# Kernel optimization log

Hardware: AMD Instinct MI355X
Metric: run time of the kernel (lower is better)

Reference implementation:

```python
import jax, jax.numpy as jnp
import numpy as np

LP, LQ, B, D0, H = 128, 128, 64, 150, 150
D = 2 * D0  # in_size after self-concatenation


def setup_inputs() -> dict:
    key = jax.random.key(0)
    ks = jax.random.split(key, 12)
    s = 0.08  # weight scale to keep tanh/sigmoid out of hard saturation
    return {
        "Up": jax.random.normal(ks[0], (LP, B, D0), jnp.float32),
        "Uq": jax.random.normal(ks[1], (LQ, B, D0), jnp.float32),
        "Wp": jax.random.normal(ks[2], (H, D), jnp.float32) * s,
        "Wq": jax.random.normal(ks[3], (H, D), jnp.float32) * s,
        "Wv": jax.random.normal(ks[4], (H, H), jnp.float32) * s,
        "Wg": jax.random.normal(ks[5], (2 * D, 2 * D), jnp.float32) * s,
        "V": jax.random.normal(ks[6], (B, H), jnp.float32) * s,
        "v0": jax.random.normal(ks[7], (B, H), jnp.float32) * s,
        "W_ih": jax.random.normal(ks[8], (3 * H, 2 * D), jnp.float32) * s,
        "W_hh": jax.random.normal(ks[9], (3 * H, H), jnp.float32) * s,
        "b_ih": jax.random.normal(ks[10], (3 * H,), jnp.float32) * s,
        "b_hh": jax.random.normal(ks[11], (3 * H,), jnp.float32) * s,
    }


def reference(Up, Uq, Wp, Wq, Wv, Wg, V, v0, W_ih, W_hh, b_ih, b_hh):
    # self-concat of features, as in the original forward
    Upc = jnp.concatenate([Up, Up], axis=2)  # (LP, B, D)
    Uqc = jnp.concatenate([Uq, Uq], axis=2)  # (LQ, B, D)
    # Wq @ Uq is loop-invariant in the original; hoist it (same math)
    Wuq = jnp.einsum('lbd,hd->lbh', Uqc, Wq)  # (LQ, B, H)

    def step(v, up_i):
        # up_i: (B, D); v: (B, H)
        wup = up_i @ Wp.T                                   # (B, H)
        x = jnp.tanh(wup[None] + Wuq + (v @ Wv.T)[None])    # (LQ, B, H)
        s = jnp.einsum('lbh,bh->bl', x, V)                  # (B, LQ)
        a = jax.nn.softmax(s, axis=1)
        c = jnp.einsum('bl,lbd->bd', a, Uqc)                # (B, D)
        r = jnp.concatenate([up_i, c], axis=1)              # (B, 2D)
        r = jax.nn.sigmoid(r @ Wg.T) * r                    # gated input
        # PyTorch GRUCell math
        gi = r @ W_ih.T + b_ih                              # (B, 3H)
        gh = v @ W_hh.T + b_hh                              # (B, 3H)
        i_r, i_z, i_n = jnp.split(gi, 3, axis=1)
        h_r, h_z, h_n = jnp.split(gh, 3, axis=1)
        rr = jax.nn.sigmoid(i_r + h_r)
        zz = jax.nn.sigmoid(i_z + h_z)
        n = jnp.tanh(i_n + rr * h_n)
        h = (1.0 - zz) * n + zz * v
        return h, h

    _, vs = jax.lax.scan(step, v0, Upc)  # vs: (LP, B, H)
    return vs  # dropout in eval mode = identity
```

## Files before the change

kernel.cpp:

```cpp
#include <hip/hip_runtime.h>
#include <hip/hip_fp16.h>

typedef _Float16 h2_t __attribute__((ext_vector_type(2)));

__device__ __forceinline__ float dot2f(int w, int x, float acc) {
#if __has_builtin(__builtin_amdgcn_fdot2)
  return __builtin_amdgcn_fdot2(__builtin_bit_cast(h2_t, w),
                                __builtin_bit_cast(h2_t, x), acc, false);
#else
  h2_t a = __builtin_bit_cast(h2_t, w);
  h2_t b = __builtin_bit_cast(h2_t, x);
  return acc + (float)a[0] * (float)b[0] + (float)a[1] * (float)b[1];
#endif
}

__device__ __forceinline__ float rcp_f(float x) {
#if __has_builtin(__builtin_amdgcn_rcpf)
  return __builtin_amdgcn_rcpf(x);
#else
  return 1.0f / x;
#endif
}

__device__ __forceinline__ float fast_tanh(float x) {
  float e = exp2f(x * 2.885390082f);
  return 1.0f - 2.0f * rcp_f(e + 1.0f);
}
__device__ __forceinline__ float fast_sigmoid(float x) {
  return rcp_f(1.0f + exp2f(x * -1.442695041f));
}
__device__ __forceinline__ int packh2(float a, float b) {
  h2_t h;
  h[0] = (_Float16)a;
  h[1] = (_Float16)b;
  return __builtin_bit_cast(int, h);
}

__device__ __forceinline__ int ldi_coh(const int* p) {
  return __hip_atomic_load((int*)p, __ATOMIC_RELAXED, __HIP_MEMORY_SCOPE_AGENT);
}
__device__ __forceinline__ float ldf_coh(const float* p) {
  return __hip_atomic_load((float*)p, __ATOMIC_RELAXED,
                           __HIP_MEMORY_SCOPE_AGENT);
}
__device__ __forceinline__ void sti_coh(int* p, int v) {
  __hip_atomic_store(p, v, __ATOMIC_RELAXED, __HIP_MEMORY_SCOPE_AGENT);
}
__device__ __forceinline__ void stf_coh(float* p, float v) {
  __hip_atomic_store(p, v, __ATOMIC_RELAXED, __HIP_MEMORY_SCOPE_AGENT);
}

#define DOTC(W, X, A)                                                          \
  {                                                                            \
    int4 _x = (X);                                                             \
    A = dot2f((W).x, _x.x, A);                                                 \
    A = dot2f((W).y, _x.y, A);                                                 \
    A = dot2f((W).z, _x.z, A);                                                 \
    A = dot2f((W).w, _x.w, A);                                                 \
  }

__global__ void prep_weights(const float* __restrict__ Wp,
                             const float* __restrict__ Wv,
                             const float* __restrict__ Wg,
                             const float* __restrict__ Wih,
                             const float* __restrict__ Whh,
                             __half* __restrict__ oMa, __half* __restrict__ oWg,
                             __half* __restrict__ oWih,
                             __half* __restrict__ oWhh, int* __restrict__ flags,
                             int* __restrict__ payload) {
  if (blockIdx.x == 0) {
    for (int j = threadIdx.x; j < 1024; j += 256) flags[j] = 0;
  }
  if (blockIdx.x == 1 && threadIdx.x < 384) {
    int cc = threadIdx.x / 6, s = threadIdx.x % 6;
    int off;
    if (s < 2)
      off = 150 + s;
    else if (s < 4)
      off = 160 + 150 + (s - 2);
    else
      off = 160 + 302 + (s - 4);
    payload[cc * 2048 + off] = 0;
  }
  int idx = blockIdx.x * 256 + threadIdx.x;
  const int NMa = 150 * 304, NWg = 600 * 304, NWih = 900 * 304,
            NWhh = 452 * 152;
  if (idx < NMa) {
    int r = idx / 304, c = idx % 304;
    float v = 0.f;
    if (c < 150)
      v = Wp[r * 300 + c] + Wp[r * 300 + 150 + c];
    else if (c >= 152 && c < 302)
      v = Wv[r * 150 + (c - 152)];
    oMa[(c >> 3) * 1200 + r * 8 + (c & 7)] = __float2half(v);
    return;
  }
  idx -= NMa;
  if (idx < NWg) {
    int r = idx / 304, c = idx % 304;
    float v = 0.f;
    if (c < 150)
      v = Wg[r * 600 + c] + Wg[r * 600 + 150 + c];
    else if (c >= 152 && c < 302) {
      int d = c - 152;
      v = Wg[r * 600 + 300 + d] + Wg[r * 600 + 450 + d];
    }
    oWg[(c >> 3) * 4800 + r * 8 + (c & 7)] = __float2half(v);
    return;
  }
  idx -= NWg;
  if (idx < NWih) {
    int s = idx / 304, c = idx % 304;
    int r = s >> 1, off = (s & 1) * 300;
    float v = (c < 300) ? Wih[r * 600 + off + c] : 0.f;
    oWih[(c >> 3) * 7200 + s * 8 + (c & 7)] = __float2half(v);
    return;
  }
  idx -= NWih;
  if (idx < NWhh) {
    int r = idx / 152, c = idx % 152;
    float v = (r < 450 && c < 150) ? Whh[r * 150 + c] : 0.f;
    oWhh[(c >> 3) * 3616 + r * 8 + (c & 7)] = __float2half(v);
  }
}

__global__ __launch_bounds__(256) void prep_wuq(const float* __restrict__ Uq,
                                                const float* __restrict__ Wq,
                                                __half* __restrict__ oWuq,
                                                __half* __restrict__ oUqh) {
  __shared__ float sUql[64 * 150];
  const int l = blockIdx.x, tid = threadIdx.x;
  for (int idx = tid; idx < 9600; idx += 256) sUql[idx] = Uq[l * 9600 + idx];
  __syncthreads();
  for (int idx = tid; idx < 64 * 152; idx += 256) {
    int bb = idx / 152, d = idx % 152;
    float v = (d < 150) ? sUql[bb * 150 + d] : 0.f;
    oUqh[(size_t)bb * 19456 + l * 152 + d] = __float2half(v);
  }
  if (tid < 152) {
    const int h = tid;
    if (h < 150) {
      float wq[150];
#pragma unroll
      for (int d = 0; d < 150; ++d)
        wq[d] = Wq[h * 300 + d] + Wq[h * 300 + 150 + d];
      for (int bb = 0; bb < 64; ++bb) {
        float acc = 0.f;
#pragma unroll
        for (int d = 0; d < 150; ++d) acc += wq[d] * sUql[bb * 150 + d];
        oWuq[(size_t)bb * 19456 + l * 152 + h] = __float2half(acc);
      }
    } else {
      for (int bb = 0; bb < 64; ++bb)
        oWuq[(size_t)bb * 19456 + l * 152 + h] = __float2half(0.f);
    }
  }
}

__device__ __forceinline__ void post_and_wait(int* f4, int q, int target) {
  __syncthreads();
  if (threadIdx.x == 0) sti_coh(&f4[q], target);
  if (threadIdx.x < 4) {
    int spins = 0;
    while (ldi_coh(&f4[threadIdx.x]) < target && ++spins < (1 << 20)) {
    }
  }
  __syncthreads();
}

__global__ __launch_bounds__(1024, 1) void pq_main(
    const float* __restrict__ Up, const float* __restrict__ V,
    const float* __restrict__ v0, const float* __restrict__ b_ih,
    const float* __restrict__ b_hh, const int* __restrict__ gWuq,
    const __half* __restrict__ gUqh, const int* __restrict__ gMa,
    const int* __restrict__ gWg, const int* __restrict__ gWih,
    const int* __restrict__ gWhh, int* __restrict__ flags,
    int* __restrict__ payload, float* __restrict__ out) {
  __shared__ __align__(16) float sTV[304];
  __shared__ __align__(16) float sV[152];
  __shared__ __align__(16) float sGh[456];
  __shared__ __align__(16) float sS[128];
  __shared__ __align__(16) float sC0[152];
  __shared__ __align__(16) float sCp[608];
  __shared__ __align__(16) float sU[152];
  __shared__ __align__(16) float sv_[152];
  __shared__ __align__(16) int sXd[152];
  __shared__ __align__(16) int svh[76];
  __shared__ __align__(16) int sRgh[304];
  __shared__ __align__(16) float sGi[456];
  __shared__ __align__(16) float sBih[456];
  __shared__ __align__(16) float sBhh[456];
  extern __shared__ __align__(16) int dynlds[];
  int* sWuq = dynlds;
  __half* sUqh = (__half*)(dynlds + 9728);

  const int t = threadIdx.x;
  const int c = blockIdx.x & 63;
  const int q = blockIdx.x >> 6;
  const int b = c;

  int* myflags = flags + c * 16;
  int* pl = payload + c * 2048;
  float* plT = (float*)pl;
  int* plR = pl + 160;
  float* plGi = (float*)(pl + 512);
  float* plGh = (float*)(pl + 1024);

  const int4* MaT4 = (const int4*)gMa;
  const int4* WgT4 = (const int4*)gWg;
  const int4* WihT4 = (const int4*)gWih;
  const int4* WhhT4 = (const int4*)gWhh;

  const int baseR = 113 * q - (q == 3 ? 1 : 0);
  const int cntR = (q < 2) ? 113 : 112;

  int4 a0, a1, a2, a3, a4, a5, a6, a7, a8, a9;
  int4 b0, b1, b2, b3, b4, b5, b6, b7, b8, b9;
  {
    const int4* p;
    int nr, sub, step, nch, row;
    if (t < 152) {
      p = MaT4; nr = 150; step = 4; nch = 38;
      sub = t & 3; row = 38 * q + (t >> 2);
      if (row > 149) row = 149;
    } else if (t < 378) {
      p = WhhT4; nr = 452; step = 2; nch = 19;
      int u2 = t - 152; sub = u2 & 1; row = baseR + (u2 >> 1);
    } else if (t >= 384 && t < 984) {
      p = WgT4; nr = 600; step = 4; nch = 38;
      int u2 = t - 384; sub = u2 & 3; row = 150 * q + (u2 >> 2);
    } else {
      p = MaT4; nr = 150; step = 4; nch = 38; sub = 0; row = 0;
    }
#define LDA(i)                                                                 \
  {                                                                            \
    int cc = sub + step * (i);                                                 \
    if (cc > nch - 1) cc = nch - 1;                                            \
    a##i = p[cc * nr + row];                                                   \
  }
    LDA(0) LDA(1) LDA(2) LDA(3) LDA(4) LDA(5) LDA(6) LDA(7) LDA(8) LDA(9)
#undef LDA
  }
  {
    int rl = t >> 3, oct = t & 7;
    int row = baseR + rl;
    if (rl >= cntR || t >= 904) row = baseR;
#define LDB(i)                                                                 \
  {                                                                            \
    int c8 = oct + 8 * (i);                                                    \
    if (c8 > 75) c8 = 75;                                                      \
    int hf = (c8 >= 38) ? 1 : 0;                                               \
    int cc = c8 - 38 * hf;                                                     \
    b##i = WihT4[cc * 900 + 2 * row + hf];                                     \
  }
    LDB(0) LDB(1) LDB(2) LDB(3) LDB(4) LDB(5) LDB(6) LDB(7) LDB(8) LDB(9)
#undef LDB
  }

  for (int idx = t; idx < 9728; idx += 1024) sWuq[idx] = gWuq[b * 9728 + idx];
  {
    const int* gU2 = (const int*)(gUqh + (size_t)b * 19456);
    int* sU2 = (int*)sUqh;
    for (int idx = t; idx < 9728; idx += 1024) sU2[idx] = gU2[idx];
  }
  if (t < 150) {
    sV[t] = V[b * 150 + t];
    float v_ = v0[b * 150 + t];
    sv_[t] = v_;
    float vn = __shfl_down(v_, 1);
    if (!(t & 1)) svh[t >> 1] = packh2(v_, vn);
    float u_ = Up[b * 150 + t];
    sU[t] = u_;
    float un = __shfl_down(u_, 1);
    if (!(t & 1)) sXd[t >> 1] = packh2(u_, un);
  }
  for (int idx = t; idx < 450; idx += 1024) {
    sBih[idx] = b_ih[idx];
    sBhh[idx] = b_hh[idx];
  }
  if (t == 0) {
    svh[75] = 0;
    sXd[75] = 0;
    sXd[151] = 0;
    sV[150] = 0.f;
    sV[151] = 0.f;
  }
  const int4* sXd4 = (const int4*)sXd;
  const int4* svh4 = (const int4*)svh;
  const int4* sRgh4 = (const int4*)sRgh;
  const int c_lq = t / 150;
  const int c_d0 = t - c_lq * 150;
  __syncthreads();

#pragma unroll 1
  for (int i = 0; i < 128; ++i) {
    float unext = 0.f;
    if (t >= 640 && t < 790) {
      int ii = (i < 127) ? (i + 1) : 127;
      unext = Up[ii * 9600 + b * 150 + (t - 640)];
    }

    if (t < 152) {
      int rl = t >> 2, sub = t & 3;
      int h = 38 * q + rl;
      float acc = 0.f;
#define MAD(i2)                                                                \
  {                                                                            \
    int cc = sub + 4 * (i2);                                                   \
    if (cc < 38) {                                                             \
      int4 x = (cc < 19) ? sXd4[cc] : svh4[cc - 19];                           \
      DOTC(a##i2, x, acc)                                                      \
    }                                                                          \
  }
      MAD(0) MAD(1) MAD(2) MAD(3) MAD(4) MAD(5) MAD(6) MAD(7) MAD(8) MAD(9)
#undef MAD
      acc += __shfl_xor(acc, 1);
      acc += __shfl_xor(acc, 2);
      if (sub == 0 && h < 150) stf_coh(&plT[h], acc);
    } else if (t < 378) {
      int u2 = t - 152;
      int rl = u2 >> 1, sub = u2 & 1;
      int r = baseR + rl;
      float acc = 0.f;
#define HHD(i2)                                                                \
  {                                                                            \
    int cc = sub + 2 * (i2);                                                   \
    if (cc < 19) DOTC(a##i2, svh4[cc], acc)                                    \
  }
      HHD(0) HHD(1) HHD(2) HHD(3) HHD(4) HHD(5) HHD(6) HHD(7) HHD(8) HHD(9)
#undef HHD
      acc += __shfl_xor(acc, 1);
      if (sub == 0 && rl < cntR) stf_coh(&plGh[r], acc + sBhh[r]);
    }
    post_and_wait(myflags, q, i + 1);
    if (t < 76) {
      float x0 = ldf_coh(&plT[2 * t]);
      float x1 = ldf_coh(&plT[2 * t + 1]);
      float4 tv;
      tv.x = x0;
      tv.y = x1;
      tv.z = sV[2 * t];
      tv.w = sV[2 * t + 1];
      ((float4*)sTV)[t] = tv;
    } else if (t >= 128 && t < 578) {
      sGh[t - 128] = ldf_coh(&plGh[t - 128]);
    }
    __syncthreads();

    {
      const int l = t >> 3, sub = t & 7;
      const int base = l * 76;
      const int niter = (sub < 3) ? 10 : 9;
      float acc = 0.f;
#pragma unroll
      for (int k = 0; k < 10; ++k) {
        if (k < niter) {
          int w = sub + 8 * k;
          int qq = sWuq[base + w];
          float4 tv = ((const float4*)sTV)[w];
          h2_t hq = __builtin_bit_cast(h2_t, qq);
          float x0 = (float)hq[0] + tv.x;
          float x1 = (float)hq[1] + tv.y;
          acc += fast_tanh(x0) * tv.z;
          acc += fast_tanh(x1) * tv.w;
        }
      }
      acc += __shfl_xor(acc, 1);
      acc += __shfl_xor(acc, 2);
      acc += __shfl_xor(acc, 4);
      if (sub == 0) sS[l] = acc;
    }
    __syncthreads();

    if (t < 64) {
      float s0 = sS[t], s1 = sS[t + 64];
      float m = fmaxf(s0, s1);
#pragma unroll
      for (int o = 1; o < 64; o <<= 1) m = fmaxf(m, __shfl_xor(m, o));
      float e0 = exp2f((s0 - m) * 1.442695041f);
      float e1 = exp2f((s1 - m) * 1.442695041f);
      float sum = e0 + e1;
#pragma unroll
      for (int o = 1; o < 64; o <<= 1) sum += __shfl_xor(sum, o);
      float inv = rcp_f(sum);
      sS[t] = e0 * inv;
      sS[t + 64] = e1 * inv;
    }
    __syncthreads();

    if (t < 600) {
      const __half* src = sUqh + c_lq * 32 * 152 + c_d0;
      float acc = 0.f;
#pragma unroll
      for (int j = 0; j < 32; ++j) {
        float a = sS[c_lq * 32 + j];
        acc += a * __half2float(src[j * 152]);
      }
      sCp[c_lq * 152 + c_d0] = acc;
    }
    __syncthreads();
    if (t < 150) {
      float c0 = sCp[t] + sCp[152 + t] + sCp[304 + t] + sCp[456 + t];
      sC0[t] = c0;
      float cn = __shfl_down(c0, 1);
      if (!(t & 1)) sXd[76 + (t >> 1)] = packh2(c0, cn);
    }
    __syncthreads();

    if (t >= 384 && t < 984) {
      int u2 = t - 384;
      int rl = u2 >> 2, sub = u2 & 3;
      int j = 150 * q + rl;
      float acc = 0.f;
#define WGD(i2)                                                                \
  {                                                                            \
    int cc = sub + 4 * (i2);                                                   \
    if (cc < 38) DOTC(a##i2, sXd4[cc], acc)                                    \
  }
      WGD(0) WGD(1) WGD(2) WGD(3) WGD(4) WGD(5) WGD(6) WGD(7) WGD(8) WGD(9)
#undef WGD
      acc += __shfl_xor(acc, 1);
      acc += __shfl_xor(acc, 2);
      float rb;
      if (j < 150)
        rb = sU[j];
      else if (j < 300)
        rb = sU[j - 150];
      else if (j < 450)
        rb = sC0[j - 300];
      else
        rb = sC0[j - 450];
      float rg = rb * fast_sigmoid(acc);
      float rgn = __shfl_down(rg, 4);
      if (sub == 0 && !(rl & 1)) {
        int pi = ((j < 300) ? j : (j + 4)) >> 1;
        sti_coh(&plR[pi], packh2(rg, rgn));
      }
    }
    post_and_wait(myflags + 4, q, i + 1);
    if (t < 304) sRgh[t] = ldi_coh(&plR[t]);
    __syncthreads();

    if (t < 904) {
      int rl = t >> 3, oct = t & 7;
      int r = baseR + rl;
      if (rl < cntR) {
        float acc = 0.f;
#define IHD(i2)                                                                \
  {                                                                            \
    int c8 = oct + 8 * (i2);                                                   \
    if (c8 < 76) DOTC(b##i2, sRgh4[c8], acc)                                   \
  }
        IHD(0) IHD(1) IHD(2) IHD(3) IHD(4) IHD(5) IHD(6) IHD(7) IHD(8) IHD(9)
#undef IHD
        acc += __shfl_xor(acc, 1);
        acc += __shfl_xor(acc, 2);
        acc += __shfl_xor(acc, 4);
        if (oct == 0) stf_coh(&plGi[r], acc + sBih[r]);
      }
    }
    post_and_wait(myflags + 8, q, i + 1);
    if (t < 450) sGi[t] = ldf_coh(&plGi[t]);
    __syncthreads();

    if (t < 150) {
      float ir = sGi[t], iz = sGi[150 + t], in_ = sGi[300 + t];
      float hr = sGh[t], hz = sGh[150 + t], hn = sGh[300 + t];
      float rr = fast_sigmoid(ir + hr);
      float zz = fast_sigmoid(iz + hz);
      float nn = fast_tanh(in_ + rr * hn);
      float vold = sv_[t];
      float hv = nn + zz * (vold - nn);
      if (q == 0) out[i * 9600 + b * 150 + t] = hv;
      sv_[t] = hv;
      float hv1 = __shfl_down(hv, 1);
      if (!(t & 1)) svh[t >> 1] = packh2(hv, hv1);
    } else if (t >= 640 && t < 790) {
      int t2 = t - 640;
      sU[t2] = unext;
      float un = __shfl_down(unext, 1);
      if (!(t2 & 1)) sXd[t2 >> 1] = packh2(unext, un);
    }
    __syncthreads();
  }
}

extern "C" void kernel_launch(void* const* d_in, const int* in_sizes, int n_in,
                              void* d_out, int out_size, void* d_ws,
                              size_t ws_size, hipStream_t stream) {
  const float* Up = (const float*)d_in[0];
  const float* Uq = (const float*)d_in[1];
  const float* Wp = (const float*)d_in[2];
  const float* Wq = (const float*)d_in[3];
  const float* Wv = (const float*)d_in[4];
  const float* Wg = (const float*)d_in[5];
  const float* V = (const float*)d_in[6];
  const float* v0 = (const float*)d_in[7];
  const float* Wih = (const float*)d_in[8];
  const float* Whh = (const float*)d_in[9];
  const float* bih = (const float*)d_in[10];
  const float* bhh = (const float*)d_in[11];

  char* ws = (char*)d_ws;
  __half* wsWuq = (__half*)(ws);
  __half* wsUqh = (__half*)(ws + 2490368);
  __half* wsMa = (__half*)(ws + 4980736);
  __half* wsWg = (__half*)(ws + 5071936);
  __half* wsWih = (__half*)(ws + 5436736);
  __half* wsWhh = (__half*)(ws + 5983936);
  int* wsFlags = (int*)(ws + 6121472);
  int* wsPayload = (int*)(ws + 6125568);

  (void)hipFuncSetAttribute((const void*)pq_main,
                            hipFuncAttributeMaxDynamicSharedMemorySize, 77824);

  prep_weights<<<2228, 256, 0, stream>>>(Wp, Wv, Wg, Wih, Whh, wsMa, wsWg,
                                         wsWih, wsWhh, wsFlags, wsPayload);
  prep_wuq<<<128, 256, 0, stream>>>(Uq, Wq, wsWuq, wsUqh);
  pq_main<<<256, 1024, 77824, stream>>>(Up, V, v0, bih, bhh, (const int*)wsWuq,
                                        wsUqh, (const int*)wsMa,
                                        (const int*)wsWg, (const int*)wsWih,
                                        (const int*)wsWhh, wsFlags, wsPayload,
                                        (float*)d_out);
}
```

Measured before the change: 1.486 ms.

## Split W_ih GEMV by input columns per block to drop one cross-block barrier

Each of the four cooperating blocks now computes a partial W_ih product over its own slice of the gated-input columns for all 450 rows, using only locally produced gated inputs kept in shared memory. The partials are written to the payload and summed with the bias after a single flag exchange. This removes one inter-block post/wait round trip per timestep, along with the exchange of the packed gated vector. In return each block does a larger set of reductions per step, writes four times as many partial results, and the payload buffer grows.

```diff
diff --git a/kernel.cpp b/kernel.cpp
--- a/kernel.cpp
+++ b/kernel.cpp
@@ -71,16 +71,9 @@
   if (blockIdx.x == 0) {
     for (int j = threadIdx.x; j < 1024; j += 256) flags[j] = 0;
   }
-  if (blockIdx.x == 1 && threadIdx.x < 384) {
-    int cc = threadIdx.x / 6, s = threadIdx.x % 6;
-    int off;
-    if (s < 2)
-      off = 150 + s;
-    else if (s < 4)
-      off = 160 + 150 + (s - 2);
-    else
-      off = 160 + 302 + (s - 4);
-    payload[cc * 2048 + off] = 0;
+  if (blockIdx.x == 1 && threadIdx.x < 128) {
+    int cc = threadIdx.x >> 1, s = threadIdx.x & 1;
+    payload[cc * 4096 + 150 + s] = 0;
   }
   int idx = blockIdx.x * 256 + threadIdx.x;
   const int NMa = 150 * 304, NWg = 600 * 304, NWih = 900 * 304,
@@ -200,11 +193,10 @@
   const int b = c;
 
   int* myflags = flags + c * 16;
-  int* pl = payload + c * 2048;
+  int* pl = payload + c * 4096;
   float* plT = (float*)pl;
-  int* plR = pl + 160;
-  float* plGi = (float*)(pl + 512);
-  float* plGh = (float*)(pl + 1024);
+  float* plGh = (float*)(pl + 160);
+  float* plGi = (float*)(pl + 640);
 
   const int4* MaT4 = (const int4*)gMa;
   const int4* WgT4 = (const int4*)gWg;
@@ -213,6 +205,8 @@
 
   const int baseR = 113 * q - (q == 3 ? 1 : 0);
   const int cntR = (q < 2) ? 113 : 112;
+  const int c_lo = (q == 0) ? 0 : (q == 1) ? 18 : (q == 2) ? 38 : 56;
+  const int c_hi = (q == 0) ? 18 : (q == 1) ? 37 : (q == 2) ? 56 : 75;
 
   int4 a0, a1, a2, a3, a4, a5, a6, a7, a8, a9;
   int4 b0, b1, b2, b3, b4, b5, b6, b7, b8, b9;
@@ -242,15 +236,14 @@
 #undef LDA
   }
   {
-    int rl = t >> 3, oct = t & 7;
-    int row = baseR + rl;
-    if (rl >= cntR || t >= 904) row = baseR;
+    int row = (t < 900) ? (t >> 1) : 0;
+    int sub = (t < 900) ? (t & 1) : 0;
 #define LDB(i)                                                                 \
   {                                                                            \
-    int c8 = oct + 8 * (i);                                                    \
-    if (c8 > 75) c8 = 75;                                                      \
-    int hf = (c8 >= 38) ? 1 : 0;                                               \
-    int cc = c8 - 38 * hf;                                                     \
+    int cq = c_lo + sub + 2 * (i);                                             \
+    if (cq > c_hi) cq = c_hi;                                                  \
+    int hf = (cq >= 38) ? 1 : 0;                                               \
+    int cc = cq - 38 * hf;                                                     \
     b##i = WihT4[cc * 900 + 2 * row + hf];                                     \
   }
     LDB(0) LDB(1) LDB(2) LDB(3) LDB(4) LDB(5) LDB(6) LDB(7) LDB(8) LDB(9)
@@ -278,6 +271,7 @@
     sBih[idx] = b_ih[idx];
     sBhh[idx] = b_hh[idx];
   }
+  if (t < 304) sRgh[t] = 0;
   if (t == 0) {
     svh[75] = 0;
     sXd[75] = 0;
@@ -421,46 +415,43 @@
 #undef WGD
       acc += __shfl_xor(acc, 1);
       acc += __shfl_xor(acc, 2);
-      float rb;
-      if (j < 150)
-        rb = sU[j];
-      else if (j < 300)
-        rb = sU[j - 150];
-      else if (j < 450)
-        rb = sC0[j - 300];
-      else
-        rb = sC0[j - 450];
-      float rg = rb * fast_sigmoid(acc);
-      float rgn = __shfl_down(rg, 4);
-      if (sub == 0 && !(rl & 1)) {
-        int pi = ((j < 300) ? j : (j + 4)) >> 1;
-        sti_coh(&plR[pi], packh2(rg, rgn));
+      if (sub == 0) {
+        float rb;
+        if (j < 150)
+          rb = sU[j];
+        else if (j < 300)
+          rb = sU[j - 150];
+        else if (j < 450)
+          rb = sC0[j - 300];
+        else
+          rb = sC0[j - 450];
+        float rg = rb * fast_sigmoid(acc);
+        ((__half*)sRgh)[(j < 300) ? j : (j + 4)] = __float2half(rg);
       }
     }
+    __syncthreads();
+
+    if (t < 900) {
+      int row = t >> 1, sub = t & 1;
+      float acc = 0.f;
+#define IHD(i2)                                                                \
+  {                                                                            \
+    int cq = c_lo + sub + 2 * (i2);                                            \
+    if (cq <= c_hi) DOTC(b##i2, sRgh4[cq], acc)                                \
+  }
+      IHD(0) IHD(1) IHD(2) IHD(3) IHD(4) IHD(5) IHD(6) IHD(7) IHD(8) IHD(9)
+#undef IHD
+      acc += __shfl_xor(acc, 1);
+      if (!sub) stf_coh(&plGi[456 * q + row], acc);
+    }
     post_and_wait(myflags + 4, q, i + 1);
-    if (t < 304) sRgh[t] = ldi_coh(&plR[t]);
-    __syncthreads();
-
-    if (t < 904) {
-      int rl = t >> 3, oct = t & 7;
-      int r = baseR + rl;
-      if (rl < cntR) {
-        float acc = 0.f;
-#define IHD(i2)                                                                \
-  {                                                                            \
-    int c8 = oct + 8 * (i2);                                                   \
-    if (c8 < 76) DOTC(b##i2, sRgh4[c8], acc)                                   \
-  }
-        IHD(0) IHD(1) IHD(2) IHD(3) IHD(4) IHD(5) IHD(6) IHD(7) IHD(8) IHD(9)
-#undef IHD
-        acc += __shfl_xor(acc, 1);
-        acc += __shfl_xor(acc, 2);
-        acc += __shfl_xor(acc, 4);
-        if (oct == 0) stf_coh(&plGi[r], acc + sBih[r]);
-      }
-    }
-    post_and_wait(myflags + 8, q, i + 1);
-    if (t < 450) sGi[t] = ldf_coh(&plGi[t]);
+    if (t < 450) {
+      float g0 = ldf_coh(&plGi[t]);
+      float g1 = ldf_coh(&plGi[456 + t]);
+      float g2 = ldf_coh(&plGi[912 + t]);
+      float g3 = ldf_coh(&plGi[1368 + t]);
+      sGi[t] = g0 + g1 + g2 + g3 + sBih[t];
+    }
     __syncthreads();
 
     if (t < 150) {
```

Result: faster. 1.439 ms (-3.2%).
